# Optimization experiments

Measured on AMD Instinct MI355X. Metric: run time of the kernel, lower is better.

The kernel has to match this reference:

```python
import jax, jax.numpy as jnp
import numpy as np
import math

OUT = 7   # output_size
SR = 2    # sampling_ratio


def _roi_align(feat, rois5, scale):
    """torchvision roi_align (aligned=False) for all rois against one FPN level.
    feat: [B,C,H,W], rois5: [N,5] = (batch_idx, x1, y1, x2, y2). Returns [N,C,OUT,OUT]."""
    B, C, H, W = feat.shape
    b = rois5[:, 0].astype(jnp.int32)
    x1 = rois5[:, 1] * scale
    y1 = rois5[:, 2] * scale
    x2 = rois5[:, 3] * scale
    y2 = rois5[:, 4] * scale
    rw = jnp.maximum(x2 - x1, 1.0)
    rh = jnp.maximum(y2 - y1, 1.0)
    gh = OUT * SR  # sampling grid: ph*SR+iy, sample at (g+0.5)*bin/SR from roi start
    gw = OUT * SR
    ys = y1[:, None] + (jnp.arange(gh, dtype=feat.dtype) + 0.5)[None, :] * (rh / gh)[:, None]  # [N,gh]
    xs = x1[:, None] + (jnp.arange(gw, dtype=feat.dtype) + 0.5)[None, :] * (rw / gw)[:, None]  # [N,gw]
    # torchvision bilinear_interpolate: out-of-range (< -1 or > size) -> 0, else clamp
    vy = (ys >= -1.0) & (ys <= H)
    vx = (xs >= -1.0) & (xs <= W)
    y = jnp.clip(ys, 0.0, H - 1)
    x = jnp.clip(xs, 0.0, W - 1)
    y0f = jnp.floor(y)
    x0f = jnp.floor(x)
    y0 = y0f.astype(jnp.int32)
    x0 = x0f.astype(jnp.int32)
    y1i = jnp.minimum(y0 + 1, H - 1)
    x1i = jnp.minimum(x0 + 1, W - 1)
    ly = y - y0f; hy = 1.0 - ly
    lx = x - x0f; hx = 1.0 - lx
    fT = jnp.transpose(feat, (0, 2, 3, 1))  # [B,H,W,C]

    def gather(yi, xi):
        return fT[b[:, None, None], yi[:, :, None], xi[:, None, :]]  # [N,gh,gw,C]

    w00 = (hy[:, :, None] * hx[:, None, :])[..., None]
    w01 = (hy[:, :, None] * lx[:, None, :])[..., None]
    w10 = (ly[:, :, None] * hx[:, None, :])[..., None]
    w11 = (ly[:, :, None] * lx[:, None, :])[..., None]
    val = (gather(y0, x0) * w00 + gather(y0, x1i) * w01
           + gather(y1i, x0) * w10 + gather(y1i, x1i) * w11)
    val = val * (vy[:, :, None] & vx[:, None, :])[..., None].astype(feat.dtype)
    # average SRxSR samples per output bin -> [N,OUT,OUT,C] -> [N,C,OUT,OUT]
    val = val.reshape(val.shape[0], OUT, SR, OUT, SR, C).mean(axis=(2, 4))
    return jnp.transpose(val, (0, 3, 1, 2))


def setup_inputs() -> dict:
    key = jax.random.key(0)
    ks = jax.random.split(key, 6)
    feat0 = jax.random.normal(ks[0], (2, 256, 200, 200), jnp.float32)
    feat1 = jax.random.normal(ks[1], (2, 256, 100, 100), jnp.float32)
    feat2 = jax.random.normal(ks[2], (2, 256, 50, 50), jnp.float32)
    feat3 = jax.random.normal(ks[3], (2, 256, 25, 25), jnp.float32)
    B, N = 2, 512
    xy1 = jax.random.uniform(ks[4], (B, N, 2), jnp.float32, 0.0, 700.0)
    wh = jax.random.uniform(ks[5], (B, N, 2), jnp.float32, 16.0, 320.0)
    xy2 = jnp.minimum(xy1 + wh, 799.0)
    rois = jnp.concatenate([xy1, xy2], axis=-1)  # [B,N,4] = (x1,y1,x2,y2)
    return {"feat0": feat0, "feat1": feat1, "feat2": feat2, "feat3": feat3,
            "rois": rois, "image_h": 800, "image_w": 800}


def reference(feat0, feat1, feat2, feat3, rois, image_h, image_w):
    feats = [feat0, feat1, feat2, feat3]
    B, N = rois.shape[:2]
    # _convert_to_roi_format: prepend batch index column
    bcol = jnp.repeat(jnp.arange(B, dtype=rois.dtype), N)[:, None]
    rois5 = jnp.concatenate([bcol, rois.reshape(-1, 4)], axis=1)  # [B*N,5]
    # _setup_scales / _get_scales: pow-2-rounded ratio of feature H to image H (static)
    scales = [2.0 ** round(math.log2(f.shape[2] / float(image_h))) for f in feats]
    lvl_min = -math.log2(scales[0])   # 2
    lvl_max = -math.log2(scales[-1])  # 5
    # FPN level routing: k = floor(4 + log2(sqrt(area)/224)), clamped
    area = (rois5[:, 4] - rois5[:, 2]) * (rois5[:, 3] - rois5[:, 1])
    k = jnp.floor(4.0 + jnp.log2(jnp.sqrt(area) / 224.0))
    k = jnp.clip(k, lvl_min, lvl_max) - lvl_min  # in {0,1,2,3}
    out = jnp.zeros((B * N, feats[0].shape[1], OUT, OUT), feats[0].dtype)
    for lvl, (f, s) in enumerate(zip(feats, scales)):
        pooled = _roi_align(f, rois5, s)
        out = jnp.where((k == lvl)[:, None, None, None], pooled, out)
    return out
```

## Files before the change

### kernel.cpp

```cpp
#include <hip/hip_runtime.h>

#define OUTS 7
#define SR 2
#define GRIDW 14
#define NS 196
#define NCH 256
#define NROI 1024
#define NBIN 49

#define L0_OFF 0
#define L1_OFF 20480000
#define L2_OFF 25600000
#define L3_OFF 26880000
#define WS_ELEMS 27200000

static __device__ __forceinline__ unsigned short f2bf(float f) {
    unsigned u = __builtin_bit_cast(unsigned, f);
    u += 0x7fffu + ((u >> 16) & 1u);
    return (unsigned short)(u >> 16);
}

__global__ __launch_bounds__(256) void nchw_to_nhwc_bf16(
    const float* __restrict__ f0, const float* __restrict__ f1,
    const float* __restrict__ f2, const float* __restrict__ f3,
    unsigned short* __restrict__ ws) {
    __shared__ float tile[64 * 66];
    int bid = blockIdx.x;
    const float* in; unsigned short* outp; int P, ptiles, local;
    if (bid < 5000)      { in = f0; outp = ws + L0_OFF; P = 40000; ptiles = 625; local = bid; }
    else if (bid < 6256) { in = f1; outp = ws + L1_OFF; P = 10000; ptiles = 157; local = bid - 5000; }
    else if (bid < 6576) { in = f2; outp = ws + L2_OFF; P = 2500;  ptiles = 40;  local = bid - 6256; }
    else                 { in = f3; outp = ws + L3_OFF; P = 625;   ptiles = 10;  local = bid - 6576; }
    int pt = local % ptiles;
    int rest = local / ptiles;
    int c0 = (rest & 3) * 64;
    int b  = rest >> 2;
    int p0 = pt * 64;
    int t = threadIdx.x;
    int l = t & 63, w = t >> 6;

    const float* inb = in + (size_t)(b * NCH + c0) * P;
    unsigned short* outb = outp + (size_t)b * P * NCH;

    {
        int px = (l & 15) * 4;
        int p = p0 + px;
        if ((P & 3) == 0) {
#pragma unroll
            for (int i = 0; i < 4; ++i) {
                int c = w * 16 + i * 4 + (l >> 4);
                if (p < P) {
                    float4 v = *(const float4*)(inb + (size_t)c * P + p);
                    int pxs = px ^ (((c >> 2) & 7) << 2);
                    *(float2*)&tile[c * 66 + pxs]     = make_float2(v.x, v.y);
                    *(float2*)&tile[c * 66 + pxs + 2] = make_float2(v.z, v.w);
                }
            }
        } else {
#pragma unroll
            for (int i = 0; i < 4; ++i) {
                int c = w * 16 + i * 4 + (l >> 4);
                int pxs = px ^ (((c >> 2) & 7) << 2);
                const float* src = inb + (size_t)c * P;
#pragma unroll
                for (int k = 0; k < 4; ++k) {
                    tile[c * 66 + pxs + k] = (p + k < P) ? src[p + k] : 0.0f;
                }
            }
        }
    }
    __syncthreads();

    {
        int j = t & 15;
        int pb = t >> 4;
        int S = (j & 7) << 2;
#pragma unroll
        for (int it = 0; it < 4; ++it) {
            int pp = pb + it * 16;
            int p = p0 + pp;
            if (p < P) {
                int pxs = pp ^ S;
                float a0 = tile[(4 * j + 0) * 66 + pxs];
                float a1 = tile[(4 * j + 1) * 66 + pxs];
                float a2 = tile[(4 * j + 2) * 66 + pxs];
                float a3 = tile[(4 * j + 3) * 66 + pxs];
                unsigned u0 = (unsigned)f2bf(a0) | ((unsigned)f2bf(a1) << 16);
                unsigned u1 = (unsigned)f2bf(a2) | ((unsigned)f2bf(a3) << 16);
                *(uint2*)(outb + (size_t)p * NCH + c0 + 4 * j) = make_uint2(u0, u1);
            }
        }
    }
}

__global__ __launch_bounds__(256) void roi_gather_nhwc(
    const unsigned short* __restrict__ nhwc,
    const float* __restrict__ rois,
    float* __restrict__ out) {
    __shared__ int   s_off[4][NS];
    __shared__ float s_w[4][NS];
    __shared__ float lds_out[13 * 260];

    int n = blockIdx.x >> 2;
    int q = blockIdx.x & 3;
    int B0 = q * 13;
    int Bend = min(B0 + 13, NBIN);
    int ncol = Bend - B0;
    int tid = threadIdx.x;
    int b = n >> 9;

    float x1 = rois[n * 4 + 0];
    float y1 = rois[n * 4 + 1];
    float x2 = rois[n * 4 + 2];
    float y2 = rois[n * 4 + 3];
    float area = (y2 - y1) * (x2 - x1);
    float kf = floorf(4.0f + log2f(sqrtf(area) / 224.0f));
    kf = fminf(fmaxf(kf, 2.0f), 5.0f);
    int lvl = (int)kf - 2;
    float scale = ldexpf(0.25f, -lvl);
    int H, W; size_t base;
    switch (lvl) {
        case 0:  H = 200; W = 200; base = L0_OFF; break;
        case 1:  H = 100; W = 100; base = L1_OFF; break;
        case 2:  H = 50;  W = 50;  base = L2_OFF; break;
        default: H = 25;  W = 25;  base = L3_OFF; break;
    }
    float x1s = x1 * scale, y1s = y1 * scale;
    float rw = fmaxf(x2 * scale - x1s, 1.0f);
    float rh = fmaxf(y2 * scale - y1s, 1.0f);
    float sx = rw * (1.0f / GRIDW);
    float sy = rh * (1.0f / GRIDW);

    if (tid < NS) {
        int gy = tid / GRIDW, gx = tid % GRIDW;
        float y = y1s + ((float)gy + 0.5f) * sy;
        float x = x1s + ((float)gx + 0.5f) * sx;
        bool valid = (y >= -1.0f) && (y <= (float)H) && (x >= -1.0f) && (x <= (float)W);
        float yc = fminf(fmaxf(y, 0.0f), (float)(H - 1));
        float xc = fminf(fmaxf(x, 0.0f), (float)(W - 1));
        int y0 = (int)floorf(yc), x0 = (int)floorf(xc);
        int y1i = min(y0 + 1, H - 1), x1i = min(x0 + 1, W - 1);
        float ly = yc - (float)y0, lx = xc - (float)x0;
        float hy = 1.0f - ly, hx = 1.0f - lx;
        float vm = valid ? 1.0f : 0.0f;
        s_off[0][tid] = (y0 * W + x0) * NCH;
        s_off[1][tid] = (y0 * W + x1i) * NCH;
        s_off[2][tid] = (y1i * W + x0) * NCH;
        s_off[3][tid] = (y1i * W + x1i) * NCH;
        s_w[0][tid] = hy * hx * vm;
        s_w[1][tid] = hy * lx * vm;
        s_w[2][tid] = ly * hx * vm;
        s_w[3][tid] = ly * lx * vm;
    }
    __syncthreads();

    int lane = tid & 63;
    int wave = tid >> 6;
    const unsigned short* fc = nhwc + base + (size_t)b * (size_t)H * W * NCH + lane * 4;

    for (int bin = B0 + wave; bin < Bend; bin += 4) {
        int ph = bin / OUTS, pw = bin % OUTS;
        float4 acc = make_float4(0.f, 0.f, 0.f, 0.f);
#pragma unroll
        for (int iy = 0; iy < SR; ++iy) {
#pragma unroll
            for (int ix = 0; ix < SR; ++ix) {
                int s = (ph * SR + iy) * GRIDW + (pw * SR + ix);
#pragma unroll
                for (int tp = 0; tp < 4; ++tp) {
                    float wgt = s_w[tp][s];
                    uint2 v = *(const uint2*)(fc + s_off[tp][s]);
                    acc.x += wgt * __builtin_bit_cast(float, v.x << 16);
                    acc.y += wgt * __builtin_bit_cast(float, v.x & 0xffff0000u);
                    acc.z += wgt * __builtin_bit_cast(float, v.y << 16);
                    acc.w += wgt * __builtin_bit_cast(float, v.y & 0xffff0000u);
                }
            }
        }
        acc.x *= 0.25f; acc.y *= 0.25f; acc.z *= 0.25f; acc.w *= 0.25f;
        *(float4*)&lds_out[(bin - B0) * 260 + lane * 4] = acc;
    }
    __syncthreads();

    float* og = out + (size_t)n * (NCH * NBIN);
    for (int i = tid; i < 256 * 13; i += 256) {
        int c = (i * 20165) >> 18;
        int col = i - c * 13;
        if (col < ncol) og[c * NBIN + B0 + col] = lds_out[col * 260 + c];
    }
}


struct RoiMeta {
    float x1, y1, sx, sy;
    int level, b, pad0, pad1;
};

__global__ void prep_rois_kernel(const float* __restrict__ rois,
                                 RoiMeta* __restrict__ meta, int total) {
    int n = blockIdx.x * blockDim.x + threadIdx.x;
    if (n >= total) return;
    float x1 = rois[n * 4 + 0];
    float y1 = rois[n * 4 + 1];
    float x2 = rois[n * 4 + 2];
    float y2 = rois[n * 4 + 3];
    float area = (y2 - y1) * (x2 - x1);
    float k = floorf(4.0f + log2f(sqrtf(area) / 224.0f));
    k = fminf(fmaxf(k, 2.0f), 5.0f);
    int lvl = (int)k - 2;
    float scale = ldexpf(0.25f, -lvl);
    float x1s = x1 * scale;
    float y1s = y1 * scale;
    float rw = fmaxf(x2 * scale - x1s, 1.0f);
    float rh = fmaxf(y2 * scale - y1s, 1.0f);
    RoiMeta m;
    m.x1 = x1s; m.y1 = y1s;
    m.sx = rw / (float)(OUTS * SR);
    m.sy = rh / (float)(OUTS * SR);
    m.level = lvl;
    m.b = n / 512;
    m.pad0 = 0; m.pad1 = 0;
    meta[n] = m;
}

__global__ __launch_bounds__(256) void roi_align_kernel(
    const float* __restrict__ f0, const float* __restrict__ f1,
    const float* __restrict__ f2, const float* __restrict__ f3,
    const RoiMeta* __restrict__ meta, float* __restrict__ out, int total) {
    int idx = blockIdx.x * 256 + threadIdx.x;
    if (idx >= total) return;
    int pw = idx % OUTS;
    int ph = (idx / OUTS) % OUTS;
    int c  = (idx / (OUTS * OUTS)) & (NCH - 1);
    int n  = idx / (OUTS * OUTS * NCH);

    RoiMeta m = meta[n];
    const float* f; int H, W;
    switch (m.level) {
        case 0:  f = f0; H = 200; W = 200; break;
        case 1:  f = f1; H = 100; W = 100; break;
        case 2:  f = f2; H = 50;  W = 50;  break;
        default: f = f3; H = 25;  W = 25;  break;
    }
    const float* fc = f + (size_t)(m.b * NCH + c) * H * W;

    float acc = 0.0f;
#pragma unroll
    for (int iy = 0; iy < SR; ++iy) {
        float y = m.y1 + ((float)(ph * SR + iy) + 0.5f) * m.sy;
        if (y < -1.0f || y > (float)H) continue;
        float yc = fminf(fmaxf(y, 0.0f), (float)(H - 1));
        int y0 = (int)floorf(yc);
        int y1i = min(y0 + 1, H - 1);
        float ly = yc - (float)y0;
        float hy = 1.0f - ly;
        const float* r0 = fc + (size_t)y0 * W;
        const float* r1 = fc + (size_t)y1i * W;
#pragma unroll
        for (int ix = 0; ix < SR; ++ix) {
            float x = m.x1 + ((float)(pw * SR + ix) + 0.5f) * m.sx;
            if (x < -1.0f || x > (float)W) continue;
            float xc = fminf(fmaxf(x, 0.0f), (float)(W - 1));
            int x0 = (int)floorf(xc);
            int x1i = min(x0 + 1, W - 1);
            float lx = xc - (float)x0;
            float hx = 1.0f - lx;
            acc += hy * (hx * r0[x0] + lx * r0[x1i]) +
                   ly * (hx * r1[x0] + lx * r1[x1i]);
        }
    }
    out[idx] = acc * 0.25f;
}


extern "C" void kernel_launch(void* const* d_in, const int* in_sizes, int n_in,
                              void* d_out, int out_size, void* d_ws, size_t ws_size,
                              hipStream_t stream) {
    const float* f0 = (const float*)d_in[0];
    const float* f1 = (const float*)d_in[1];
    const float* f2 = (const float*)d_in[2];
    const float* f3 = (const float*)d_in[3];
    const float* rois = (const float*)d_in[4];
    float* out = (float*)d_out;

    if (ws_size >= (size_t)WS_ELEMS * sizeof(unsigned short)) {
        unsigned short* nhwc = (unsigned short*)d_ws;
        nchw_to_nhwc_bf16<<<6656, 256, 0, stream>>>(f0, f1, f2, f3, nhwc);
        roi_gather_nhwc<<<NROI * 4, 256, 0, stream>>>(nhwc, rois, out);
    } else {
        RoiMeta* meta = (RoiMeta*)d_ws;
        prep_rois_kernel<<<(NROI + 255) / 256, 256, 0, stream>>>(rois, meta, NROI);
        const int total = NROI * NCH * OUTS * OUTS;
        roi_align_kernel<<<(total + 255) / 256, 256, 0, stream>>>(
            f0, f1, f2, f3, meta, out, total);
    }
}
```

Before: 83.01 us.

## Split roi_gather blocks by channel quarter and spread bilinear taps across lanes

```diff
diff --git a/kernel.cpp b/kernel.cpp
--- a/kernel.cpp
+++ b/kernel.cpp
@@ -18,6 +18,13 @@
     unsigned u = __builtin_bit_cast(unsigned, f);
     u += 0x7fffu + ((u >> 16) & 1u);
     return (unsigned short)(u >> 16);
+}
+
+static __device__ __forceinline__ float bfhi(unsigned u) {
+    return __builtin_bit_cast(float, u & 0xffff0000u);
+}
+static __device__ __forceinline__ float bflo(unsigned u) {
+    return __builtin_bit_cast(float, u << 16);
 }
 
 __global__ __launch_bounds__(256) void nchw_to_nhwc_bf16(
@@ -99,13 +106,10 @@
     float* __restrict__ out) {
     __shared__ int   s_off[4][NS];
     __shared__ float s_w[4][NS];
-    __shared__ float lds_out[13 * 260];
+    __shared__ float lds_out[64 * 53];
 
     int n = blockIdx.x >> 2;
     int q = blockIdx.x & 3;
-    int B0 = q * 13;
-    int Bend = min(B0 + 13, NBIN);
-    int ncol = Bend - B0;
     int tid = threadIdx.x;
     int b = n >> 9;
 
@@ -156,37 +160,47 @@
 
     int lane = tid & 63;
     int wave = tid >> 6;
-    const unsigned short* fc = nhwc + base + (size_t)b * (size_t)H * W * NCH + lane * 4;
-
-    for (int bin = B0 + wave; bin < Bend; bin += 4) {
-        int ph = bin / OUTS, pw = bin % OUTS;
+    int t = lane >> 4;
+    int j = lane & 15;
+    const unsigned short* fcq =
+        nhwc + base + (size_t)b * (size_t)H * W * NCH + q * 64 + j * 4;
+
+    for (int bin = wave; bin < NBIN; bin += 4) {
+        int ph = bin / OUTS, pw = bin - ph * OUTS;
+        int sbase = (ph * SR) * GRIDW + pw * SR;
         float4 acc = make_float4(0.f, 0.f, 0.f, 0.f);
 #pragma unroll
-        for (int iy = 0; iy < SR; ++iy) {
-#pragma unroll
-            for (int ix = 0; ix < SR; ++ix) {
-                int s = (ph * SR + iy) * GRIDW + (pw * SR + ix);
-#pragma unroll
-                for (int tp = 0; tp < 4; ++tp) {
-                    float wgt = s_w[tp][s];
-                    uint2 v = *(const uint2*)(fc + s_off[tp][s]);
-                    acc.x += wgt * __builtin_bit_cast(float, v.x << 16);
-                    acc.y += wgt * __builtin_bit_cast(float, v.x & 0xffff0000u);
-                    acc.z += wgt * __builtin_bit_cast(float, v.y << 16);
-                    acc.w += wgt * __builtin_bit_cast(float, v.y & 0xffff0000u);
-                }
-            }
-        }
-        acc.x *= 0.25f; acc.y *= 0.25f; acc.z *= 0.25f; acc.w *= 0.25f;
-        *(float4*)&lds_out[(bin - B0) * 260 + lane * 4] = acc;
+        for (int k = 0; k < 4; ++k) {
+            int s = sbase + (k >> 1) * GRIDW + (k & 1);
+            float wgt = s_w[t][s];
+            uint2 v = *(const uint2*)(fcq + s_off[t][s]);
+            acc.x += wgt * bflo(v.x);
+            acc.y += wgt * bfhi(v.x);
+            acc.z += wgt * bflo(v.y);
+            acc.w += wgt * bfhi(v.y);
+        }
+        acc.x += __shfl_xor(acc.x, 16, 64);
+        acc.y += __shfl_xor(acc.y, 16, 64);
+        acc.z += __shfl_xor(acc.z, 16, 64);
+        acc.w += __shfl_xor(acc.w, 16, 64);
+        acc.x += __shfl_xor(acc.x, 32, 64);
+        acc.y += __shfl_xor(acc.y, 32, 64);
+        acc.z += __shfl_xor(acc.z, 32, 64);
+        acc.w += __shfl_xor(acc.w, 32, 64);
+        if (t == 0) {
+            lds_out[(4 * j + 0) * 53 + bin] = acc.x * 0.25f;
+            lds_out[(4 * j + 1) * 53 + bin] = acc.y * 0.25f;
+            lds_out[(4 * j + 2) * 53 + bin] = acc.z * 0.25f;
+            lds_out[(4 * j + 3) * 53 + bin] = acc.w * 0.25f;
+        }
     }
     __syncthreads();
 
-    float* og = out + (size_t)n * (NCH * NBIN);
-    for (int i = tid; i < 256 * 13; i += 256) {
-        int c = (i * 20165) >> 18;
-        int col = i - c * 13;
-        if (col < ncol) og[c * NBIN + B0 + col] = lds_out[col * 260 + c];
+    float* og = out + (size_t)n * (NCH * NBIN) + (size_t)q * 64 * NBIN;
+    for (int i = tid; i < 64 * NBIN; i += 256) {
+        int c = i / NBIN;
+        int bin = i - c * NBIN;
+        og[i] = lds_out[c * 53 + bin];
     }
 }
 
```

Result: faster. 68.12 us, median of 2 (-17.9%).
